# Optimization experiments

Hardware: AMD Instinct MI355X
Metric: run time of the kernel (lower is better)

## Reference

```python
import jax, jax.numpy as jnp
import numpy as np

N_NODES = 50000


def gcn_conv(x, W, b, row, col, num_nodes):
    """PyG-style GCNConv: out = D^{-1/2}(A+I)D^{-1/2} (x @ W) + b.

    row/col already include self-loops. x: [N, Fin], W: [Fin, Fout].
    """
    h = x @ W  # [N, Fout]
    deg = jax.ops.segment_sum(jnp.ones_like(col, dtype=h.dtype), col,
                              num_segments=num_nodes)  # in-degree incl. self-loop
    dinv = jnp.where(deg > 0, jax.lax.rsqrt(deg), 0.0)
    norm = dinv[row] * dinv[col]  # [E]
    msgs = h[row] * norm[:, None]  # gather + scale, [E, Fout]
    out = jax.ops.segment_sum(msgs, col, num_segments=num_nodes)  # scatter-add
    return out + b


def setup_inputs() -> dict:
    key = jax.random.key(0)
    k1, k2, k3, k4 = jax.random.split(key, 4)
    Fin, Fh, Fout = 128, 128, 64
    E = 800000
    x = jax.random.normal(k1, (N_NODES, Fin), dtype=jnp.float32)
    edge_index = jax.random.randint(k2, (2, E), 0, N_NODES, dtype=jnp.int64)
    # Glorot-ish init for weights
    W1 = jax.random.normal(k3, (Fin, Fh), dtype=jnp.float32) / np.sqrt(Fin)
    b1 = jnp.zeros((Fh,), dtype=jnp.float32)
    W2 = jax.random.normal(k4, (Fh, Fout), dtype=jnp.float32) / np.sqrt(Fh)
    b2 = jnp.zeros((Fout,), dtype=jnp.float32)
    return {"x": x, "edge_index": edge_index, "W1": W1, "b1": b1,
            "W2": W2, "b2": b2}


def reference(x, edge_index, W1, b1, W2, b2):
    n = x.shape[0]
    # add self-loops once (shared by both conv layers)
    loops = jnp.arange(n, dtype=edge_index.dtype)
    row = jnp.concatenate([edge_index[0], loops])
    col = jnp.concatenate([edge_index[1], loops])
    h = jax.nn.relu(gcn_conv(x, W1, b1, row, col, n))
    # dropout(p=0.5) is identity in eval mode (self.training == False)
    return gcn_conv(h, W2, b2, row, col, n)
```

## Files before the change

### kernel.cpp

```cpp
#include <hip/hip_runtime.h>


constexpr int KD = 128;
constexpr int CHUNK = 2048;
constexpr int BCAP = 6144;

using short8  = __attribute__((ext_vector_type(8))) short;
using float4v = __attribute__((ext_vector_type(4))) float;


__device__ __forceinline__ unsigned short f2bf(float f) {
    unsigned int u = __float_as_uint(f);
    u = (u + 0x7fffu + ((u >> 16) & 1u)) >> 16;
    return (unsigned short)u;
}

__device__ __forceinline__ float2 bfpair(unsigned int u) {
    float2 f;
    f.x = __uint_as_float(u << 16);
    f.y = __uint_as_float(u & 0xffff0000u);
    return f;
}

__device__ __forceinline__ unsigned int packbf(float x, float y) {
    return (unsigned int)f2bf(x) | ((unsigned int)f2bf(y) << 16);
}

__device__ __forceinline__ void bfsplit(float x, unsigned short& h, unsigned short& l) {
    h = f2bf(x);
    float fh = __uint_as_float((unsigned int)h << 16);
    l = f2bf(x - fh);
}

__global__ __launch_bounds__(256) void scatter_setup(
        const int* __restrict__ row, const int* __restrict__ col,
        int* gcur, unsigned int* __restrict__ bpack, int E, int NBS,
        const float* __restrict__ W1, unsigned short* __restrict__ Wth1,
        unsigned short* __restrict__ Wtl1,
        const float* __restrict__ W2, unsigned short* __restrict__ Wth2,
        unsigned short* __restrict__ Wtl2) {
    __shared__ int lh[256];
    __shared__ int lbase[256];

    if ((int)blockIdx.x >= NBS) {
        int id = ((int)blockIdx.x - NBS) * 256 + threadIdx.x;
        unsigned short h, l;
        if (id < 16384) {
            int k = id >> 7, n = id & 127;
            bfsplit(W1[id], h, l);
            Wth1[n * KD + k] = h;
            Wtl1[n * KD + k] = l;
        } else {
            int id2 = id - 16384;
            int k = id2 >> 6, n = id2 & 63;
            bfsplit(W2[id2], h, l);
            Wth2[n * KD + k] = h;
            Wtl2[n * KD + k] = l;
        }
        return;
    }

    lh[threadIdx.x] = 0;
    __syncthreads();
    int base = (int)blockIdx.x * CHUNK;
#pragma unroll
    for (int r = 0; r < CHUNK / 256; ++r) {
        int e = base + r * 256 + threadIdx.x;
        if (e < E) atomicAdd(&lh[col[e] >> 8], 1);
    }
    __syncthreads();
    int c0 = lh[threadIdx.x];
    lbase[threadIdx.x] = c0 ? (threadIdx.x * BCAP + atomicAdd(&gcur[threadIdx.x], c0)) : 0;
    __syncthreads();
    lh[threadIdx.x] = 0;
    __syncthreads();
#pragma unroll
    for (int r = 0; r < CHUNK / 256; ++r) {
        int e = base + r * 256 + threadIdx.x;
        if (e < E) {
            int c = col[e];
            int b = c >> 8;
            int slot = lbase[b] + atomicAdd(&lh[b], 1);
            bpack[slot] = ((unsigned int)row[e] << 16) | (unsigned int)c;
        }
    }
}

__global__ __launch_bounds__(256) void csr_and_gemm1(
        const unsigned int* __restrict__ bpack, const int* __restrict__ gcur,
        int* __restrict__ rowptr, float* __restrict__ dinv,
        unsigned short* __restrict__ srow, int N, int E, int NBUCKET,
        const float* __restrict__ X,
        const unsigned short* __restrict__ Wth,
        const unsigned short* __restrict__ Wtl,
        unsigned short* __restrict__ G) {
    __shared__ int s[256];
    __shared__ int lh[256];
    __shared__ int lcur[256];
    __shared__ int sh_bstart;

    if ((int)blockIdx.x < NBUCKET) {
        int b = blockIdx.x;
        int t = threadIdx.x;
        int cntb = gcur[t];
        s[t] = cntb;
        __syncthreads();
        for (int off = 1; off < 256; off <<= 1) {
            int tv = (t >= off) ? s[t - off] : 0;
            __syncthreads();
            s[t] += tv;
            __syncthreads();
        }
        if (t == b) sh_bstart = s[t] - cntb;
        if (b == 0 && t == 0) rowptr[N] = E;
        lh[t] = 0;
        __syncthreads();
        int bstart = sh_bstart;
        int nE = gcur[b];
        int base = b * BCAP;
        for (int i = t; i < nE; i += 256)
            atomicAdd(&lh[bpack[base + i] & 255], 1);
        __syncthreads();
        int v = lh[t];
        s[t] = v;
        __syncthreads();
        for (int off = 1; off < 256; off <<= 1) {
            int tv = (t >= off) ? s[t - off] : 0;
            __syncthreads();
            s[t] += tv;
            __syncthreads();
        }
        int myStart = bstart + s[t] - v;
        int node = (b << 8) + t;
        if (node < N) {
            rowptr[node] = myStart;
            dinv[node] = rsqrtf(1.0f + (float)v);
        }
        lcur[t] = myStart;
        __syncthreads();
        for (int i = t; i < nE; i += 256) {
            unsigned int p = bpack[base + i];
            int slot = atomicAdd(&lcur[p & 255], 1);
            srow[slot] = (unsigned short)(p >> 16);
        }
    } else {
        constexpr int FOUT = 128, NT = 8;
        int wave = threadIdx.x >> 6;
        int lane = threadIdx.x & 63;
        int row0 = (((int)blockIdx.x - NBUCKET) * 4 + wave) * 16;
        if (row0 >= N) return;
        int m = lane & 15;
        int quad = lane >> 4;

        float4v acc[NT];
#pragma unroll
        for (int ct = 0; ct < NT; ++ct) acc[ct] = (float4v){0.f, 0.f, 0.f, 0.f};

        const float* xrow = X + (size_t)(row0 + m) * KD + quad * 8;

#pragma unroll
        for (int ks = 0; ks < 4; ++ks) {
            float4 xa = *(const float4*)(xrow + ks * 32);
            float4 xb = *(const float4*)(xrow + ks * 32 + 4);
            float xs[8] = {xa.x, xa.y, xa.z, xa.w, xb.x, xb.y, xb.z, xb.w};
            short8 ah, al;
#pragma unroll
            for (int j = 0; j < 8; ++j) {
                unsigned short h, l;
                bfsplit(xs[j], h, l);
                ah[j] = (short)h;
                al[j] = (short)l;
            }
            int koff = ks * 32 + quad * 8;
#pragma unroll
            for (int ct = 0; ct < NT; ++ct) {
                short8 bh = *(const short8*)(Wth + (size_t)(ct * 16 + m) * KD + koff);
                short8 bl = *(const short8*)(Wtl + (size_t)(ct * 16 + m) * KD + koff);
                acc[ct] = __builtin_amdgcn_mfma_f32_16x16x32_bf16(ah, bh, acc[ct], 0, 0, 0);
                acc[ct] = __builtin_amdgcn_mfma_f32_16x16x32_bf16(al, bh, acc[ct], 0, 0, 0);
                acc[ct] = __builtin_amdgcn_mfma_f32_16x16x32_bf16(ah, bl, acc[ct], 0, 0, 0);
            }
        }

#pragma unroll
        for (int r = 0; r < 4; ++r) {
            int row = row0 + quad * 4 + r;
#pragma unroll
            for (int ct = 0; ct < NT; ++ct) {
                G[(size_t)row * FOUT + ct * 16 + m] = f2bf(acc[ct][r]);
            }
        }
    }
}

__global__ __launch_bounds__(256) void gemm_mfma2(const unsigned short* __restrict__ H,
                                                  const unsigned short* __restrict__ Wth,
                                                  const unsigned short* __restrict__ Wtl,
                                                  const float* __restrict__ dinv,
                                                  unsigned short* __restrict__ G, int N) {
    constexpr int FOUT = 64, NT = 4;
    int wave = threadIdx.x >> 6;
    int lane = threadIdx.x & 63;
    int row0 = (blockIdx.x * 4 + wave) * 16;
    if (row0 >= N) return;
    int m = lane & 15;
    int quad = lane >> 4;

    float4v acc[NT];
#pragma unroll
    for (int ct = 0; ct < NT; ++ct) acc[ct] = (float4v){0.f, 0.f, 0.f, 0.f};

    const unsigned short* hrow = H + (size_t)(row0 + m) * KD + quad * 8;

#pragma unroll
    for (int ks = 0; ks < 4; ++ks) {
        short8 a = *(const short8*)(hrow + ks * 32);
        int koff = ks * 32 + quad * 8;
#pragma unroll
        for (int ct = 0; ct < NT; ++ct) {
            short8 bh = *(const short8*)(Wth + (size_t)(ct * 16 + m) * KD + koff);
            short8 bl = *(const short8*)(Wtl + (size_t)(ct * 16 + m) * KD + koff);
            acc[ct] = __builtin_amdgcn_mfma_f32_16x16x32_bf16(a, bh, acc[ct], 0, 0, 0);
            acc[ct] = __builtin_amdgcn_mfma_f32_16x16x32_bf16(a, bl, acc[ct], 0, 0, 0);
        }
    }

#pragma unroll
    for (int r = 0; r < 4; ++r) {
        int row = row0 + quad * 4 + r;
        float s = dinv[row];
#pragma unroll
        for (int ct = 0; ct < 4; ++ct) {
            G[(size_t)row * FOUT + ct * 16 + m] = f2bf(acc[ct][r] * s);
        }
    }
}

template <bool RELU>
__global__ __launch_bounds__(256) void gather128(const int* __restrict__ rowptr,
                                                 const unsigned short* __restrict__ srow,
                                                 const unsigned int* __restrict__ G,
                                                 const float* __restrict__ dinv,
                                                 const float* __restrict__ bias,
                                                 unsigned int* __restrict__ H2,
                                                 int N, int E) {
    int tid = blockIdx.x * 256 + (int)threadIdx.x;
    int node = tid >> 5;
    int lane = threadIdx.x & 63;
    int l32 = lane & 31;
    bool valid = node < N;
    int nc = valid ? node : (N - 1);
    int beg = rowptr[nc];
    int end = rowptr[nc + 1];
    int deg = valid ? (end - beg) : 0;
    float dn = dinv[nc];

    uint2 s0 = ((const uint2*)G)[(size_t)nc * 32 + l32];
    float2 p0 = bfpair(s0.x), p1 = bfpair(s0.y);
    float ax = p0.x * dn, ay = p0.y * dn, az = p1.x * dn, aw = p1.y * dn;

    int degmax = max(deg, __shfl_xor(deg, 32));

    for (int w = 0; w < degmax; w += 32) {
        int li = w + l32;
        li = (li < deg) ? li : (deg > 0 ? deg - 1 : 0);
        li += beg;
        li = (li < E) ? li : (E - 1);
        int rv = (int)srow[li];
        float dv = dinv[rv];
        int lim = degmax - w;
        for (int g = 0; g < 32 && g < lim; g += 8) {
            uint2 u[8];
            float dr[8];
#pragma unroll
            for (int j = 0; j < 8; ++j) {
                int src = (lane & 32) | (g + j);
                int r = __shfl(rv, src);
                dr[j] = __shfl(dv, src);
                u[j] = ((const uint2*)G)[(size_t)r * 32 + l32];
            }
            float sx = 0.f, sy = 0.f, sz = 0.f, sw = 0.f;
#pragma unroll
            for (int j = 0; j < 8; ++j) {
                bool ok = (w + g + j) < deg;
                unsigned int ux = ok ? u[j].x : 0u;
                unsigned int uy = ok ? u[j].y : 0u;
                float2 v0 = bfpair(ux), v1 = bfpair(uy);
                sx = fmaf(dr[j], v0.x, sx);
                sy = fmaf(dr[j], v0.y, sy);
                sz = fmaf(dr[j], v1.x, sz);
                sw = fmaf(dr[j], v1.y, sw);
            }
            ax += sx; ay += sy; az += sz; aw += sw;
        }
    }
    if (!valid) return;
    float4 bv = ((const float4*)bias)[l32];
    float ox = ax * dn + bv.x;
    float oy = ay * dn + bv.y;
    float oz = az * dn + bv.z;
    float ow = aw * dn + bv.w;
    if (RELU) {
        ox = fmaxf(ox, 0.f); oy = fmaxf(oy, 0.f);
        oz = fmaxf(oz, 0.f); ow = fmaxf(ow, 0.f);
    }
    unsigned long long pv =
        ((unsigned long long)packbf(oz, ow) << 32) | (unsigned long long)packbf(ox, oy);
    __builtin_nontemporal_store(pv, (unsigned long long*)H2 + (size_t)nc * 32 + l32);
}

template <bool RELU>
__global__ __launch_bounds__(256) void gather64(const int* __restrict__ rowptr,
                                                const unsigned short* __restrict__ srow,
                                                const unsigned int* __restrict__ G,
                                                const float* __restrict__ dinv,
                                                const float* __restrict__ bias,
                                                float* __restrict__ O, int N, int E) {
    int tid = blockIdx.x * 256 + (int)threadIdx.x;
    int node = tid >> 4;
    int lane = threadIdx.x & 63;
    int l16 = lane & 15;
    bool valid = node < N;
    int nc = valid ? node : (N - 1);
    int beg = rowptr[nc];
    int end = rowptr[nc + 1];
    int deg = valid ? (end - beg) : 0;

    uint2 s0 = ((const uint2*)G)[(size_t)nc * 16 + l16];
    float2 p0 = bfpair(s0.x), p1 = bfpair(s0.y);
    float ax = p0.x, ay = p0.y, az = p1.x, aw = p1.y;

    int dm = max(deg, __shfl_xor(deg, 16));
    dm = max(dm, __shfl_xor(dm, 32));

    for (int w = 0; w < dm; w += 16) {
        int li = w + l16;
        li = (li < deg) ? li : (deg > 0 ? deg - 1 : 0);
        li += beg;
        li = (li < E) ? li : (E - 1);
        int rv = (int)srow[li];
        int lim = dm - w;
        for (int g = 0; g < 16 && g < lim; g += 8) {
            uint2 u[8];
#pragma unroll
            for (int j = 0; j < 8; ++j) {
                int src = (lane & 48) | (g + j);
                int r = __shfl(rv, src);
                u[j] = ((const uint2*)G)[(size_t)r * 16 + l16];
            }
            float sx = 0.f, sy = 0.f, sz = 0.f, sw = 0.f;
#pragma unroll
            for (int j = 0; j < 8; ++j) {
                bool ok = (w + g + j) < deg;
                unsigned int ux = ok ? u[j].x : 0u;
                unsigned int uy = ok ? u[j].y : 0u;
                float2 v0 = bfpair(ux), v1 = bfpair(uy);
                sx += v0.x; sy += v0.y; sz += v1.x; sw += v1.y;
            }
            ax += sx; ay += sy; az += sz; aw += sw;
        }
    }
    if (!valid) return;
    float s = dinv[nc];
    float4 bv = ((const float4*)bias)[l16];
    float ox = ax * s + bv.x;
    float oy = ay * s + bv.y;
    float oz = az * s + bv.z;
    float ow = aw * s + bv.w;
    if (RELU) {
        ox = fmaxf(ox, 0.f); oy = fmaxf(oy, 0.f);
        oz = fmaxf(oz, 0.f); ow = fmaxf(ow, 0.f);
    }
    float4v o = {ox, oy, oz, ow};
    __builtin_nontemporal_store(o, (float4v*)O + (size_t)nc * 16 + l16);
}

extern "C" void kernel_launch(void* const* d_in, const int* in_sizes, int n_in,
                              void* d_out, int out_size, void* d_ws, size_t ws_size,
                              hipStream_t stream) {
    const float* x  = (const float*)d_in[0];
    const int*   ei = (const int*)d_in[1];
    const float* W1 = (const float*)d_in[2];
    const float* b1 = (const float*)d_in[3];
    const float* W2 = (const float*)d_in[4];
    const float* b2 = (const float*)d_in[5];
    float* out = (float*)d_out;

    int N = in_sizes[0] / 128;
    int E = in_sizes[1] / 2;
    const int* row = ei;
    const int* col = ei + E;

    char* ws = (char*)d_ws;
    float* dinv   = (float*)(ws + 0x000000);
    int*   rowptr = (int*)  (ws + 0x080000);
    int*   gcur   = (int*)  (ws + 0x0F9000);
    unsigned short* srow = (unsigned short*)(ws + 0x100000);
    unsigned short* g1 = (unsigned short*)(ws + 0x440000);
    unsigned short* wth1 = (unsigned short*)(ws + 0x10C0000);
    unsigned short* wtl1 = (unsigned short*)(ws + 0x10D0000);
    unsigned short* wth2 = (unsigned short*)(ws + 0x10E0000);
    unsigned short* wtl2 = (unsigned short*)(ws + 0x10F0000);
    unsigned short* h2 = (unsigned short*)(ws + 0x1200000);
    unsigned short* g2 = (unsigned short*)(ws + 0x2C00000);
    unsigned int* bpack = (unsigned int*)(ws + 0x1200000);

    int NB_BKT  = (E + CHUNK - 1) / CHUNK;
    int NBUCKET = (N + 255) / 256;
    int NB_GEMM1 = (N + 63) / 64;
    int NB_SETUP = 96;

    hipMemsetAsync(gcur, 0, 256 * sizeof(int), stream);
    scatter_setup<<<NB_BKT + NB_SETUP, 256, 0, stream>>>(
        row, col, gcur, bpack, E, NB_BKT, W1, wth1, wtl1, W2, wth2, wtl2);
    csr_and_gemm1<<<NBUCKET + NB_GEMM1, 256, 0, stream>>>(
        bpack, gcur, rowptr, dinv, srow, N, E, NBUCKET, x, wth1, wtl1, g1);

    int nb;
    nb = (N + 7) / 8;
    gather128<true><<<nb, 256, 0, stream>>>(rowptr, srow, (const unsigned int*)g1,
                                            dinv, b1, (unsigned int*)h2, N, E);

    nb = (N + 63) / 64;
    gemm_mfma2<<<nb, 256, 0, stream>>>(h2, wth2, wtl2, dinv, g2, N);
    nb = (N + 15) / 16;
    gather64<false><<<nb, 256, 0, stream>>>(rowptr, srow, (const unsigned int*)g2,
                                            dinv, b2, out, N, E);
}
```

Before: 194.3 us.

## Bucket nodes by in-degree into a permutation to balance gather warps

The CSR build now places each node into a degree-specific slot range of a permutation array, with capacities sized on the host from a Poisson estimate of the degree distribution and an overflow region. Both gather kernels iterate over permutation slots instead of node ids, so the half-wave pairs sharing a loop have similar degrees and waste fewer idle iterations. The inner gather batch also shrinks from 8 to 4 loads. Costs are padded empty slots, extra atomics, a memset of the permutation, an indirection load per node, and less coalesced output writes; capacities assume roughly uniform random edges.

```diff
diff --git a/kernel.cpp b/kernel.cpp
--- a/kernel.cpp
+++ b/kernel.cpp
@@ -1,9 +1,13 @@
 #include <hip/hip_runtime.h>
+#include <cmath>
 
 
 constexpr int KD = 128;
 constexpr int CHUNK = 2048;
 constexpr int BCAP = 6144;
+constexpr int NDEG = 48;
+
+struct DegCaps { int base[NDEG + 1]; int cap[NDEG]; };
 
 using short8  = __attribute__((ext_vector_type(8))) short;
 using float4v = __attribute__((ext_vector_type(4))) float;
@@ -93,7 +97,8 @@
         const float* __restrict__ X,
         const unsigned short* __restrict__ Wth,
         const unsigned short* __restrict__ Wtl,
-        unsigned short* __restrict__ G) {
+        unsigned short* __restrict__ G,
+        DegCaps dc, int* __restrict__ pcnt, unsigned short* __restrict__ perm) {
     __shared__ int s[256];
     __shared__ int lh[256];
     __shared__ int lcur[256];
@@ -135,6 +140,15 @@
         if (node < N) {
             rowptr[node] = myStart;
             dinv[node] = rsqrtf(1.0f + (float)v);
+            int slot;
+            if (v < NDEG) {
+                int off = atomicAdd(&pcnt[v], 1);
+                slot = (off < dc.cap[v]) ? (dc.base[v] + off)
+                                         : (dc.base[NDEG] + atomicAdd(&pcnt[NDEG], 1));
+            } else {
+                slot = dc.base[NDEG] + atomicAdd(&pcnt[NDEG], 1);
+            }
+            perm[slot] = (unsigned short)node;
         }
         lcur[t] = myStart;
         __syncthreads();
@@ -237,19 +251,20 @@
 }
 
 template <bool RELU>
-__global__ __launch_bounds__(256) void gather128(const int* __restrict__ rowptr,
+__global__ __launch_bounds__(256) void gather128(const unsigned short* __restrict__ perm,
+                                                 const int* __restrict__ rowptr,
                                                  const unsigned short* __restrict__ srow,
                                                  const unsigned int* __restrict__ G,
                                                  const float* __restrict__ dinv,
                                                  const float* __restrict__ bias,
                                                  unsigned int* __restrict__ H2,
-                                                 int N, int E) {
-    int tid = blockIdx.x * 256 + (int)threadIdx.x;
-    int node = tid >> 5;
+                                                 int N, int E, int CAPTOT) {
+    int slot = (blockIdx.x * 256 + (int)threadIdx.x) >> 5;
     int lane = threadIdx.x & 63;
     int l32 = lane & 31;
+    int node = (slot < CAPTOT) ? (int)perm[slot] : 0xFFFF;
     bool valid = node < N;
-    int nc = valid ? node : (N - 1);
+    int nc = valid ? node : 0;
     int beg = rowptr[nc];
     int end = rowptr[nc + 1];
     int deg = valid ? (end - beg) : 0;
@@ -269,11 +284,11 @@
         int rv = (int)srow[li];
         float dv = dinv[rv];
         int lim = degmax - w;
-        for (int g = 0; g < 32 && g < lim; g += 8) {
-            uint2 u[8];
-            float dr[8];
-#pragma unroll
-            for (int j = 0; j < 8; ++j) {
+        for (int g = 0; g < 32 && g < lim; g += 4) {
+            uint2 u[4];
+            float dr[4];
+#pragma unroll
+            for (int j = 0; j < 4; ++j) {
                 int src = (lane & 32) | (g + j);
                 int r = __shfl(rv, src);
                 dr[j] = __shfl(dv, src);
@@ -281,7 +296,7 @@
             }
             float sx = 0.f, sy = 0.f, sz = 0.f, sw = 0.f;
 #pragma unroll
-            for (int j = 0; j < 8; ++j) {
+            for (int j = 0; j < 4; ++j) {
                 bool ok = (w + g + j) < deg;
                 unsigned int ux = ok ? u[j].x : 0u;
                 unsigned int uy = ok ? u[j].y : 0u;
@@ -310,18 +325,20 @@
 }
 
 template <bool RELU>
-__global__ __launch_bounds__(256) void gather64(const int* __restrict__ rowptr,
+__global__ __launch_bounds__(256) void gather64(const unsigned short* __restrict__ perm,
+                                                const int* __restrict__ rowptr,
                                                 const unsigned short* __restrict__ srow,
                                                 const unsigned int* __restrict__ G,
                                                 const float* __restrict__ dinv,
                                                 const float* __restrict__ bias,
-                                                float* __restrict__ O, int N, int E) {
-    int tid = blockIdx.x * 256 + (int)threadIdx.x;
-    int node = tid >> 4;
+                                                float* __restrict__ O, int N, int E,
+                                                int CAPTOT) {
+    int slot = (blockIdx.x * 256 + (int)threadIdx.x) >> 4;
     int lane = threadIdx.x & 63;
     int l16 = lane & 15;
+    int node = (slot < CAPTOT) ? (int)perm[slot] : 0xFFFF;
     bool valid = node < N;
-    int nc = valid ? node : (N - 1);
+    int nc = valid ? node : 0;
     int beg = rowptr[nc];
     int end = rowptr[nc + 1];
     int deg = valid ? (end - beg) : 0;
@@ -340,17 +357,17 @@
         li = (li < E) ? li : (E - 1);
         int rv = (int)srow[li];
         int lim = dm - w;
-        for (int g = 0; g < 16 && g < lim; g += 8) {
-            uint2 u[8];
-#pragma unroll
-            for (int j = 0; j < 8; ++j) {
+        for (int g = 0; g < 16 && g < lim; g += 4) {
+            uint2 u[4];
+#pragma unroll
+            for (int j = 0; j < 4; ++j) {
                 int src = (lane & 48) | (g + j);
                 int r = __shfl(rv, src);
                 u[j] = ((const uint2*)G)[(size_t)r * 16 + l16];
             }
             float sx = 0.f, sy = 0.f, sz = 0.f, sw = 0.f;
 #pragma unroll
-            for (int j = 0; j < 8; ++j) {
+            for (int j = 0; j < 4; ++j) {
                 bool ok = (w + g + j) < deg;
                 unsigned int ux = ok ? u[j].x : 0u;
                 unsigned int uy = ok ? u[j].y : 0u;
@@ -395,7 +412,9 @@
     float* dinv   = (float*)(ws + 0x000000);
     int*   rowptr = (int*)  (ws + 0x080000);
     int*   gcur   = (int*)  (ws + 0x0F9000);
+    int*   pcnt   = gcur + 256;
     unsigned short* srow = (unsigned short*)(ws + 0x100000);
+    unsigned short* perm = (unsigned short*)(ws + 0x300000);
     unsigned short* g1 = (unsigned short*)(ws + 0x440000);
     unsigned short* wth1 = (unsigned short*)(ws + 0x10C0000);
     unsigned short* wtl1 = (unsigned short*)(ws + 0x10D0000);
@@ -405,25 +424,42 @@
     unsigned short* g2 = (unsigned short*)(ws + 0x2C00000);
     unsigned int* bpack = (unsigned int*)(ws + 0x1200000);
 
+    DegCaps dc;
+    double lam = (double)E / (double)N;
+    double p = exp(-lam);
+    int acc = 0;
+    for (int d = 0; d < NDEG; ++d) {
+        dc.base[d] = acc;
+        dc.cap[d] = (int)((double)N * p) + 384;
+        acc += dc.cap[d];
+        p *= lam / (double)(d + 1);
+    }
+    dc.base[NDEG] = acc;
+    int CAPTOT = acc + 4096;
+
     int NB_BKT  = (E + CHUNK - 1) / CHUNK;
     int NBUCKET = (N + 255) / 256;
     int NB_GEMM1 = (N + 63) / 64;
     int NB_SETUP = 96;
 
-    hipMemsetAsync(gcur, 0, 256 * sizeof(int), stream);
+    hipMemsetAsync(gcur, 0, (256 + 64) * sizeof(int), stream);
+    hipMemsetAsync(perm, 0xFF, (size_t)CAPTOT * sizeof(unsigned short), stream);
     scatter_setup<<<NB_BKT + NB_SETUP, 256, 0, stream>>>(
         row, col, gcur, bpack, E, NB_BKT, W1, wth1, wtl1, W2, wth2, wtl2);
     csr_and_gemm1<<<NBUCKET + NB_GEMM1, 256, 0, stream>>>(
-        bpack, gcur, rowptr, dinv, srow, N, E, NBUCKET, x, wth1, wtl1, g1);
+        bpack, gcur, rowptr, dinv, srow, N, E, NBUCKET, x, wth1, wtl1, g1,
+        dc, pcnt, perm);
 
     int nb;
-    nb = (N + 7) / 8;
-    gather128<true><<<nb, 256, 0, stream>>>(rowptr, srow, (const unsigned int*)g1,
-                                            dinv, b1, (unsigned int*)h2, N, E);
+    nb = (CAPTOT + 7) / 8;
+    gather128<true><<<nb, 256, 0, stream>>>(perm, rowptr, srow,
+                                            (const unsigned int*)g1,
+                                            dinv, b1, (unsigned int*)h2, N, E, CAPTOT);
 
     nb = (N + 63) / 64;
     gemm_mfma2<<<nb, 256, 0, stream>>>(h2, wth2, wtl2, dinv, g2, N);
-    nb = (N + 15) / 16;
-    gather64<false><<<nb, 256, 0, stream>>>(rowptr, srow, (const unsigned int*)g2,
-                                            dinv, b2, out, N, E);
-}
+    nb = (CAPTOT + 15) / 16;
+    gather64<false><<<nb, 256, 0, stream>>>(perm, rowptr, srow,
+                                            (const unsigned int*)g2,
+                                            dinv, b2, out, N, E, CAPTOT);
+}
```

New measurement: 322.9 us. +66.2%, slower.

## Fuse layer-1 aggregation with layer-2 GEMM through shared memory

Applied to the files above, without the earlier changes.

Merges the layer-1 gather/ReLU kernel and the layer-2 MFMA GEMM into one kernel. Each block aggregates 16 nodes into LDS as bf16 and then multiplies that tile by W2 with MFMA. This removes the h2 round trip through global memory and one kernel launch. The gather now uses 16 lanes per node with 128-bit loads instead of 32 lanes with 64-bit loads, which changes load width and the per-lane latency chain. A block-wide barrier now makes each block wait for its slowest node before the GEMM.

```diff
diff --git a/kernel.cpp b/kernel.cpp
--- a/kernel.cpp
+++ b/kernel.cpp
@@ -7,6 +7,7 @@
 
 using short8  = __attribute__((ext_vector_type(8))) short;
 using float4v = __attribute__((ext_vector_type(4))) float;
+using uint4v  = __attribute__((ext_vector_type(4))) unsigned int;
 
 
 __device__ __forceinline__ unsigned short f2bf(float f) {
@@ -193,120 +194,123 @@
     }
 }
 
-__global__ __launch_bounds__(256) void gemm_mfma2(const unsigned short* __restrict__ H,
-                                                  const unsigned short* __restrict__ Wth,
-                                                  const unsigned short* __restrict__ Wtl,
-                                                  const float* __restrict__ dinv,
-                                                  unsigned short* __restrict__ G, int N) {
-    constexpr int FOUT = 64, NT = 4;
-    int wave = threadIdx.x >> 6;
+__global__ __launch_bounds__(256) void gather128_gemm2(
+        const int* __restrict__ rowptr,
+        const unsigned short* __restrict__ srow,
+        const unsigned int* __restrict__ G,
+        const float* __restrict__ dinv,
+        const float* __restrict__ bias,
+        const unsigned short* __restrict__ Wth,
+        const unsigned short* __restrict__ Wtl,
+        unsigned short* __restrict__ G2,
+        int N, int E) {
+    __shared__ unsigned int lhs[16 * 64];
+    __shared__ float ldinv[16];
+
     int lane = threadIdx.x & 63;
-    int row0 = (blockIdx.x * 4 + wave) * 16;
-    if (row0 >= N) return;
-    int m = lane & 15;
-    int quad = lane >> 4;
-
-    float4v acc[NT];
-#pragma unroll
-    for (int ct = 0; ct < NT; ++ct) acc[ct] = (float4v){0.f, 0.f, 0.f, 0.f};
-
-    const unsigned short* hrow = H + (size_t)(row0 + m) * KD + quad * 8;
-
-#pragma unroll
-    for (int ks = 0; ks < 4; ++ks) {
-        short8 a = *(const short8*)(hrow + ks * 32);
-        int koff = ks * 32 + quad * 8;
-#pragma unroll
-        for (int ct = 0; ct < NT; ++ct) {
-            short8 bh = *(const short8*)(Wth + (size_t)(ct * 16 + m) * KD + koff);
-            short8 bl = *(const short8*)(Wtl + (size_t)(ct * 16 + m) * KD + koff);
-            acc[ct] = __builtin_amdgcn_mfma_f32_16x16x32_bf16(a, bh, acc[ct], 0, 0, 0);
-            acc[ct] = __builtin_amdgcn_mfma_f32_16x16x32_bf16(a, bl, acc[ct], 0, 0, 0);
-        }
-    }
-
-#pragma unroll
-    for (int r = 0; r < 4; ++r) {
-        int row = row0 + quad * 4 + r;
-        float s = dinv[row];
-#pragma unroll
-        for (int ct = 0; ct < 4; ++ct) {
-            G[(size_t)row * FOUT + ct * 16 + m] = f2bf(acc[ct][r] * s);
-        }
-    }
-}
-
-template <bool RELU>
-__global__ __launch_bounds__(256) void gather128(const int* __restrict__ rowptr,
-                                                 const unsigned short* __restrict__ srow,
-                                                 const unsigned int* __restrict__ G,
-                                                 const float* __restrict__ dinv,
-                                                 const float* __restrict__ bias,
-                                                 unsigned int* __restrict__ H2,
-                                                 int N, int E) {
-    int tid = blockIdx.x * 256 + (int)threadIdx.x;
-    int node = tid >> 5;
-    int lane = threadIdx.x & 63;
-    int l32 = lane & 31;
+    int l16 = threadIdx.x & 15;
+    int q = threadIdx.x >> 4;
+    int node = (int)blockIdx.x * 16 + q;
     bool valid = node < N;
-    int nc = valid ? node : (N - 1);
+    int nc = valid ? node : 0;
     int beg = rowptr[nc];
     int end = rowptr[nc + 1];
     int deg = valid ? (end - beg) : 0;
     float dn = dinv[nc];
-
-    uint2 s0 = ((const uint2*)G)[(size_t)nc * 32 + l32];
-    float2 p0 = bfpair(s0.x), p1 = bfpair(s0.y);
-    float ax = p0.x * dn, ay = p0.y * dn, az = p1.x * dn, aw = p1.y * dn;
-
-    int degmax = max(deg, __shfl_xor(deg, 32));
-
-    for (int w = 0; w < degmax; w += 32) {
-        int li = w + l32;
+    if (l16 == 0) ldinv[q] = dn;
+
+    const uint4v* Gv = (const uint4v*)G;
+
+    uint4v s0 = Gv[(size_t)nc * 16 + l16];
+    float ac[8];
+    {
+        float2 v0 = bfpair(s0[0]), v1 = bfpair(s0[1]);
+        float2 v2 = bfpair(s0[2]), v3 = bfpair(s0[3]);
+        ac[0] = v0.x * dn; ac[1] = v0.y * dn;
+        ac[2] = v1.x * dn; ac[3] = v1.y * dn;
+        ac[4] = v2.x * dn; ac[5] = v2.y * dn;
+        ac[6] = v3.x * dn; ac[7] = v3.y * dn;
+    }
+
+    int dm = max(deg, __shfl_xor(deg, 16));
+    dm = max(dm, __shfl_xor(dm, 32));
+
+    for (int w = 0; w < dm; w += 16) {
+        int li = w + l16;
         li = (li < deg) ? li : (deg > 0 ? deg - 1 : 0);
         li += beg;
         li = (li < E) ? li : (E - 1);
         int rv = (int)srow[li];
         float dv = dinv[rv];
-        int lim = degmax - w;
-        for (int g = 0; g < 32 && g < lim; g += 8) {
-            uint2 u[8];
-            float dr[8];
-#pragma unroll
-            for (int j = 0; j < 8; ++j) {
-                int src = (lane & 32) | (g + j);
+        int lim = dm - w;
+        for (int g = 0; g < 16 && g < lim; g += 4) {
+            uint4v u[4];
+            float dr[4];
+#pragma unroll
+            for (int j = 0; j < 4; ++j) {
+                int src = (lane & 48) | (g + j);
                 int r = __shfl(rv, src);
                 dr[j] = __shfl(dv, src);
-                u[j] = ((const uint2*)G)[(size_t)r * 32 + l32];
-            }
-            float sx = 0.f, sy = 0.f, sz = 0.f, sw = 0.f;
-#pragma unroll
-            for (int j = 0; j < 8; ++j) {
+                u[j] = Gv[(size_t)r * 16 + l16];
+            }
+            float s[8] = {0.f, 0.f, 0.f, 0.f, 0.f, 0.f, 0.f, 0.f};
+#pragma unroll
+            for (int j = 0; j < 4; ++j) {
                 bool ok = (w + g + j) < deg;
-                unsigned int ux = ok ? u[j].x : 0u;
-                unsigned int uy = ok ? u[j].y : 0u;
-                float2 v0 = bfpair(ux), v1 = bfpair(uy);
-                sx = fmaf(dr[j], v0.x, sx);
-                sy = fmaf(dr[j], v0.y, sy);
-                sz = fmaf(dr[j], v1.x, sz);
-                sw = fmaf(dr[j], v1.y, sw);
-            }
-            ax += sx; ay += sy; az += sz; aw += sw;
-        }
-    }
-    if (!valid) return;
-    float4 bv = ((const float4*)bias)[l32];
-    float ox = ax * dn + bv.x;
-    float oy = ay * dn + bv.y;
-    float oz = az * dn + bv.z;
-    float ow = aw * dn + bv.w;
-    if (RELU) {
-        ox = fmaxf(ox, 0.f); oy = fmaxf(oy, 0.f);
-        oz = fmaxf(oz, 0.f); ow = fmaxf(ow, 0.f);
-    }
-    unsigned long long pv =
-        ((unsigned long long)packbf(oz, ow) << 32) | (unsigned long long)packbf(ox, oy);
-    __builtin_nontemporal_store(pv, (unsigned long long*)H2 + (size_t)nc * 32 + l32);
+#pragma unroll
+                for (int c = 0; c < 4; ++c) {
+                    unsigned int uv = ok ? u[j][c] : 0u;
+                    float2 v = bfpair(uv);
+                    s[2 * c]     = fmaf(dr[j], v.x, s[2 * c]);
+                    s[2 * c + 1] = fmaf(dr[j], v.y, s[2 * c + 1]);
+                }
+            }
+#pragma unroll
+            for (int c = 0; c < 8; ++c) ac[c] += s[c];
+        }
+    }
+
+    {
+        float4 bv0 = ((const float4*)bias)[l16 * 2];
+        float4 bv1 = ((const float4*)bias)[l16 * 2 + 1];
+        float o[8];
+        o[0] = ac[0] * dn + bv0.x; o[1] = ac[1] * dn + bv0.y;
+        o[2] = ac[2] * dn + bv0.z; o[3] = ac[3] * dn + bv0.w;
+        o[4] = ac[4] * dn + bv1.x; o[5] = ac[5] * dn + bv1.y;
+        o[6] = ac[6] * dn + bv1.z; o[7] = ac[7] * dn + bv1.w;
+#pragma unroll
+        for (int c = 0; c < 8; ++c) o[c] = fmaxf(o[c], 0.f);
+        int lb = q * 64 + l16 * 4;
+        lhs[lb + 0] = packbf(o[0], o[1]);
+        lhs[lb + 1] = packbf(o[2], o[3]);
+        lhs[lb + 2] = packbf(o[4], o[5]);
+        lhs[lb + 3] = packbf(o[6], o[7]);
+    }
+    __syncthreads();
+
+    int ct = threadIdx.x >> 6;
+    int m = lane & 15;
+    int quad = lane >> 4;
+
+    float4v acc = (float4v){0.f, 0.f, 0.f, 0.f};
+#pragma unroll
+    for (int ks = 0; ks < 4; ++ks) {
+        short8 a = *(const short8*)&lhs[m * 64 + ks * 16 + quad * 4];
+        int koff = ks * 32 + quad * 8;
+        short8 bh = *(const short8*)(Wth + (size_t)(ct * 16 + m) * KD + koff);
+        short8 bl = *(const short8*)(Wtl + (size_t)(ct * 16 + m) * KD + koff);
+        acc = __builtin_amdgcn_mfma_f32_16x16x32_bf16(a, bh, acc, 0, 0, 0);
+        acc = __builtin_amdgcn_mfma_f32_16x16x32_bf16(a, bl, acc, 0, 0, 0);
+    }
+
+#pragma unroll
+    for (int r = 0; r < 4; ++r) {
+        int rr = quad * 4 + r;
+        int gnode = (int)blockIdx.x * 16 + rr;
+        if (gnode < N) {
+            G2[(size_t)gnode * 64 + ct * 16 + m] = f2bf(acc[r] * ldinv[rr]);
+        }
+    }
 }
 
 template <bool RELU>
@@ -401,9 +405,8 @@
     unsigned short* wtl1 = (unsigned short*)(ws + 0x10D0000);
     unsigned short* wth2 = (unsigned short*)(ws + 0x10E0000);
     unsigned short* wtl2 = (unsigned short*)(ws + 0x10F0000);
-    unsigned short* h2 = (unsigned short*)(ws + 0x1200000);
+    unsigned int* bpack = (unsigned int*)(ws + 0x1200000);
     unsigned short* g2 = (unsigned short*)(ws + 0x2C00000);
-    unsigned int* bpack = (unsigned int*)(ws + 0x1200000);
 
     int NB_BKT  = (E + CHUNK - 1) / CHUNK;
     int NBUCKET = (N + 255) / 256;
@@ -417,12 +420,10 @@
         bpack, gcur, rowptr, dinv, srow, N, E, NBUCKET, x, wth1, wtl1, g1);
 
     int nb;
-    nb = (N + 7) / 8;
-    gather128<true><<<nb, 256, 0, stream>>>(rowptr, srow, (const unsigned int*)g1,
-                                            dinv, b1, (unsigned int*)h2, N, E);
-
-    nb = (N + 63) / 64;
-    gemm_mfma2<<<nb, 256, 0, stream>>>(h2, wth2, wtl2, dinv, g2, N);
+    nb = (N + 15) / 16;
+    gather128_gemm2<<<nb, 256, 0, stream>>>(rowptr, srow, (const unsigned int*)g1,
+                                            dinv, b1, wth2, wtl2, g2, N, E);
+
     nb = (N + 15) / 16;
     gather64<false><<<nb, 256, 0, stream>>>(rowptr, srow, (const unsigned int*)g2,
                                             dinv, b2, out, N, E);
```

New measurement: 182.6 us. -6.0%, faster.
